# Optimization experiments

Hardware: AMD Instinct MI355X
Metric: run time of the kernel (lower is better)

Reference implementation:

```python
import jax, jax.numpy as jnp
import numpy as np

COST_CLASS = 1.0
COST_BBOX = 5.0
B, Q, NCLS, DBOX, T = 16, 2048, 2, 6, 1024


def setup_inputs() -> dict:
    key = jax.random.key(0)
    k1, k2, k3, k4 = jax.random.split(key, 4)
    return {
        "pred_logits": jax.random.normal(k1, (B, Q, NCLS), dtype=jnp.float32),
        "pred_boxes": jax.random.uniform(k2, (B, Q, DBOX), dtype=jnp.float32),
        "tgt_labels": jax.random.randint(k3, (T,), 0, NCLS, dtype=jnp.int64),
        "tgt_boxes": jax.random.uniform(k4, (T, DBOX), dtype=jnp.float32),
    }


def reference(pred_logits, pred_boxes, tgt_labels, tgt_boxes):
    # Faithful to HungarianMatcher.forward up to the dense cost matrix C.
    # (The final scipy linear_sum_assignment is a host-side sequential step
    # with no dense-kernel surface; C is the kernel-relevant output.)
    bs, num_queries = pred_logits.shape[:2]
    out_prob = jax.nn.softmax(pred_logits.reshape(bs * num_queries, -1), axis=-1)  # (BQ, 2)
    out_bbox = pred_boxes.reshape(bs * num_queries, -1)                            # (BQ, 6)
    # -out_prob[:, tgt_ids] -> gather target-class prob per (query, target) pair
    cost_class = -out_prob[:, tgt_labels]                                          # (BQ, T)
    # torch.cdist(p=1): L1 distance between every query box and every target box
    cost_bbox = jnp.sum(jnp.abs(out_bbox[:, None, :] - tgt_boxes[None, :, :]), axis=-1)  # (BQ, T)
    C = COST_BBOX * cost_bbox + COST_CLASS * cost_class
    return C.reshape(bs, num_queries, -1)  # (B, Q, T)
```

## Files before the change

kernel.cpp:

```cpp
#include <hip/hip_runtime.h>
#include <hip/hip_bf16.h>

#define BB     16
#define QQ     2048
#define NCLS   2
#define DBOX   6
#define TT     1024
#define ROWS   (BB * QQ)
#define TPB    256
#define TPT    4
#define RPB    16

__global__ __launch_bounds__(TPB) void hungarian_cost_kernel(
    const float* __restrict__ logits,
    const float* __restrict__ boxes,
    const int*   __restrict__ labels,
    const float* __restrict__ tboxes,
    float*       __restrict__ out)
{
    const int tid = threadIdx.x;
    const int t0  = tid * TPT;

    float tb[TPT][DBOX];
    float w[TPT];
#pragma unroll
    for (int j = 0; j < TPT; ++j) {
        const int t = t0 + j;
#pragma unroll
        for (int d = 0; d < DBOX; ++d) tb[j][d] = tboxes[t * DBOX + d];
        w[j] = (float)labels[t];
    }

    const int row0 = blockIdx.x * RPB;

#pragma unroll 1
    for (int r = 0; r < RPB; ++r) {
        const int row = row0 + r;

        const float l0  = logits[row * NCLS + 0];
        const float l1  = logits[row * NCLS + 1];
        const float e0  = __expf(l0);
        const float e1  = __expf(l1);
        const float inv = 1.0f / (e0 + e1);
        const float p0  = e0 * inv;
        const float d10 = (e1 - e0) * inv;

        float qb[DBOX];
#pragma unroll
        for (int d = 0; d < DBOX; ++d) qb[d] = boxes[row * DBOX + d];

        float c[TPT];
#pragma unroll
        for (int j = 0; j < TPT; ++j) {
            float s = 0.0f;
#pragma unroll
            for (int d = 0; d < DBOX; ++d) s += fabsf(qb[d] - tb[j][d]);
            c[j] = 5.0f * s - (p0 + w[j] * d10);
        }

        float4 v = make_float4(c[0], c[1], c[2], c[3]);
        *reinterpret_cast<float4*>(out + (size_t)row * TT + t0) = v;
    }
}

extern "C" void kernel_launch(void* const* d_in, const int* in_sizes, int n_in,
                              void* d_out, int out_size, void* d_ws, size_t ws_size,
                              hipStream_t stream) {
    const float* logits = (const float*)d_in[0];
    const float* boxes  = (const float*)d_in[1];
    const int*   labels = (const int*)  d_in[2];
    const float* tboxes = (const float*)d_in[3];
    float*       out    = (float*)d_out;

    const int grid = ROWS / RPB;
    hungarian_cost_kernel<<<grid, TPB, 0, stream>>>(logits, boxes, labels, tboxes, out);
}
```

Measured before the change: 146.5 us.

## Batch row loads in chunks and use nontemporal stores for cost output

Processes rows in chunks of four, loading logits and boxes for all rows in a chunk before computing, to expose more memory-level parallelism. Output writes use nontemporal stores to avoid polluting caches with the large streaming result. Rows per block double, halving the grid size, which may reduce occupancy-driven latency hiding.

```diff
diff --git a/kernel.cpp b/kernel.cpp
--- a/kernel.cpp
+++ b/kernel.cpp
@@ -9,7 +9,10 @@
 #define ROWS   (BB * QQ)
 #define TPB    256
 #define TPT    4
-#define RPB    16
+#define RPB    32
+#define RCHUNK 4
+
+typedef float v4f __attribute__((ext_vector_type(4)));
 
 __global__ __launch_bounds__(TPB) void hungarian_cost_kernel(
     const float* __restrict__ logits,
@@ -34,32 +37,42 @@
     const int row0 = blockIdx.x * RPB;
 
 #pragma unroll 1
-    for (int r = 0; r < RPB; ++r) {
-        const int row = row0 + r;
-
-        const float l0  = logits[row * NCLS + 0];
-        const float l1  = logits[row * NCLS + 1];
-        const float e0  = __expf(l0);
-        const float e1  = __expf(l1);
-        const float inv = 1.0f / (e0 + e1);
-        const float p0  = e0 * inv;
-        const float d10 = (e1 - e0) * inv;
-
-        float qb[DBOX];
+    for (int rc = 0; rc < RPB; rc += RCHUNK) {
+        float l0v[RCHUNK], l1v[RCHUNK], qb[RCHUNK][DBOX];
 #pragma unroll
-        for (int d = 0; d < DBOX; ++d) qb[d] = boxes[row * DBOX + d];
-
-        float c[TPT];
+        for (int r = 0; r < RCHUNK; ++r) {
+            const int row = row0 + rc + r;
+            l0v[r] = logits[row * NCLS + 0];
+            l1v[r] = logits[row * NCLS + 1];
 #pragma unroll
-        for (int j = 0; j < TPT; ++j) {
-            float s = 0.0f;
-#pragma unroll
-            for (int d = 0; d < DBOX; ++d) s += fabsf(qb[d] - tb[j][d]);
-            c[j] = 5.0f * s - (p0 + w[j] * d10);
+            for (int d = 0; d < DBOX; ++d) qb[r][d] = boxes[row * DBOX + d];
         }
 
-        float4 v = make_float4(c[0], c[1], c[2], c[3]);
-        *reinterpret_cast<float4*>(out + (size_t)row * TT + t0) = v;
+        float p0v[RCHUNK], d10v[RCHUNK];
+#pragma unroll
+        for (int r = 0; r < RCHUNK; ++r) {
+            const float e0  = __expf(l0v[r]);
+            const float e1  = __expf(l1v[r]);
+            const float inv = 1.0f / (e0 + e1);
+            p0v[r]  = e0 * inv;
+            d10v[r] = (e1 - e0) * inv;
+        }
+
+#pragma unroll
+        for (int r = 0; r < RCHUNK; ++r) {
+            const int row = row0 + rc + r;
+            float c[TPT];
+#pragma unroll
+            for (int j = 0; j < TPT; ++j) {
+                float s = 0.0f;
+#pragma unroll
+                for (int d = 0; d < DBOX; ++d) s += fabsf(qb[r][d] - tb[j][d]);
+                c[j] = 5.0f * s - (p0v[r] + w[j] * d10v[r]);
+            }
+            v4f v = { c[0], c[1], c[2], c[3] };
+            __builtin_nontemporal_store(v,
+                reinterpret_cast<v4f*>(out + (size_t)row * TT + t0));
+        }
     }
 }
 
```

Measured after the change: 155.9 us. 6.4% more time.
